# Kernel optimization log

Measured on AMD Instinct MI355X. Metric: run time of the kernel, lower is better.

The kernel has to match this reference:

```python
import jax, jax.numpy as jnp
import numpy as np

B, N, S = 8, 8192, 2048
D1, D2 = 128, 256
IN_CH = D1 + D2  # 384
MLP = [256, 128]
BN_EPS = 1e-5


def setup_inputs() -> dict:
    key = jax.random.key(0)
    ks = jax.random.split(key, 12)
    inp = {
        'xyz1': jax.random.normal(ks[0], (B, 3, N), dtype=jnp.float32),
        'xyz2': jax.random.normal(ks[1], (B, 3, S), dtype=jnp.float32),
        'points1': jax.random.normal(ks[2], (B, D1, N), dtype=jnp.float32),
        'points2': jax.random.normal(ks[3], (B, D2, S), dtype=jnp.float32),
    }
    # Conv1d(kernel=1) weights [out, in] + bias, BN gamma/beta per layer
    c_in = IN_CH
    for i, c_out in enumerate(MLP):
        scale = 1.0 / np.sqrt(c_in)
        inp[f'w{i}'] = jax.random.uniform(ks[4 + 2 * i], (c_out, c_in), jnp.float32, -scale, scale)
        inp[f'b{i}'] = jax.random.uniform(ks[5 + 2 * i], (c_out,), jnp.float32, -scale, scale)
        inp[f'g{i}'] = jnp.ones((c_out,), jnp.float32)
        inp[f'be{i}'] = jnp.zeros((c_out,), jnp.float32)
        c_in = c_out
    return inp


def _fp_forward(xyz1, xyz2, points1, points2, params):
    # xyz1: [B,3,N] -> [B,N,3]; xyz2: [B,3,S] -> [B,S,3]
    p1 = jnp.transpose(xyz1, (0, 2, 1))
    p2 = jnp.transpose(xyz2, (0, 2, 1))
    # squared pairwise distances [B,N,S]
    dist = (jnp.sum(p1 * p1, -1)[:, :, None]
            + jnp.sum(p2 * p2, -1)[:, None, :]
            - 2.0 * jnp.einsum('bnc,bsc->bns', p1, p2))
    # 3 smallest distances per query point
    neg_d, idx = jax.lax.top_k(-dist, 3)          # idx: [B,N,3]
    d3 = -neg_d
    recip = 1.0 / (d3 + 1e-8)
    weight = recip / jnp.sum(recip, axis=2, keepdims=True)  # [B,N,3]
    # gather neighbor features: points2 [B,D2,S] -> [B,S,D2]
    feats = jnp.transpose(points2, (0, 2, 1))
    gathered = feats[jnp.arange(feats.shape[0])[:, None, None], idx]  # [B,N,3,D2]
    interp = jnp.einsum('bnkd,bnk->bdn', gathered, weight)            # [B,D2,N]
    x = jnp.concatenate([points1, interp], axis=1)                    # [B,D1+D2,N]
    # Conv1d(k=1) + BatchNorm1d(train-mode batch stats) + ReLU stack
    for w, b, g, be in params:
        x = jnp.einsum('oc,bcn->bon', w, x) + b[None, :, None]
        mean = jnp.mean(x, axis=(0, 2), keepdims=True)
        var = jnp.mean((x - mean) ** 2, axis=(0, 2), keepdims=True)
        x = (x - mean) * jax.lax.rsqrt(var + BN_EPS)
        x = x * g[None, :, None] + be[None, :, None]
        x = jax.nn.relu(x)
    return x


def reference(xyz1, xyz2, points1, points2, w0, b0, g0, be0, w1, b1, g1, be1):
    params = [(w0, b0, g0, be0), (w1, b1, g1, be1)]
    return _fp_forward(xyz1, xyz2, points1, points2, params)
```

## Files before the change

kernel.cpp:

```cpp
#include <hip/hip_runtime.h>

#define NB   8
#define NPT  8192
#define NS   2048
#define ND1  128
#define ND2  256
#define NIN  384
#define NC0  256
#define NC1  128
#define NBN  (NB*NPT)

typedef __bf16 bf16x8 __attribute__((ext_vector_type(8)));
typedef __bf16 bf16x4 __attribute__((ext_vector_type(4)));
typedef float  f32x4  __attribute__((ext_vector_type(4)));

__global__ __launch_bounds__(256) void knn_kernel(
    const float* __restrict__ xyz1, const float* __restrict__ xyz2,
    int* __restrict__ idx3, float* __restrict__ wgt3)
{
    __shared__ float4 pts[NS];
    __shared__ float md[64][4][3];
    __shared__ int   mi[64][4][3];

    const int b  = blockIdx.x;
    const int qt = blockIdx.y;
    const float* x2 = xyz2 + (size_t)b * 3 * NS;
    for (int s = threadIdx.x; s < NS; s += 256) {
        float x = x2[s], y = x2[NS + s], z = x2[2 * NS + s];
        pts[s] = make_float4(x, y, z, x * x + y * y + z * z);
    }
    __syncthreads();

    const int q    = threadIdx.x & 63;
    const int part = threadIdx.x >> 6;
    const int n    = qt * 64 + q;
    const float* x1 = xyz1 + (size_t)b * 3 * NPT;
    const float px = x1[n], py = x1[NPT + n], pz = x1[2 * NPT + n];

    float d0 = 3e38f, d1 = 3e38f, d2 = 3e38f;
    int   i0 = 0, i1 = 0, i2 = 0;
    const int sbeg = part * (NS / 4);
    #pragma unroll 2
    for (int s = sbeg; s < sbeg + NS / 4; ++s) {
        float4 p = pts[s];
        float t = px * p.x;
        t = fmaf(py, p.y, t);
        t = fmaf(pz, p.z, t);
        float d = fmaf(-2.f, t, p.w);
        bool c0 = d < d0, c1 = d < d1, c2 = d < d2;
        i2 = c1 ? i1 : (c2 ? s : i2);
        i1 = c0 ? i0 : (c1 ? s : i1);
        i0 = c0 ? s  : i0;
        d2 = fminf(fmaxf(d, d1), d2);
        d1 = fminf(fmaxf(d, d0), d1);
        d0 = fminf(d, d0);
    }
    md[q][part][0] = d0; md[q][part][1] = d1; md[q][part][2] = d2;
    mi[q][part][0] = i0; mi[q][part][1] = i1; mi[q][part][2] = i2;
    __syncthreads();

    if (threadIdx.x < 64) {
        int hp[4] = {0, 0, 0, 0};
        float rd[3]; int ri[3];
        #pragma unroll
        for (int k = 0; k < 3; ++k) {
            float best = 3.0e38f; int bl = 0;
            #pragma unroll
            for (int l = 0; l < 4; ++l) {
                float dv = md[q][l][hp[l]];
                if (dv < best) { best = dv; bl = l; }
            }
            rd[k] = best; ri[k] = mi[q][bl][hp[bl]]; hp[bl]++;
        }
        const float p1sq = px * px + py * py + pz * pz;
        float r0 = 1.0f / (rd[0] + p1sq + 1e-8f);
        float r1 = 1.0f / (rd[1] + p1sq + 1e-8f);
        float r2 = 1.0f / (rd[2] + p1sq + 1e-8f);
        float inv = 1.0f / (r0 + r1 + r2);
        size_t base = ((size_t)b * NPT + n) * 3;
        idx3[base] = ri[0]; idx3[base + 1] = ri[1]; idx3[base + 2] = ri[2];
        wgt3[base] = r0 * inv; wgt3[base + 1] = r1 * inv; wgt3[base + 2] = r2 * inv;
    }
}

__global__ __launch_bounds__(256) void transpose_p2_kernel(
    const float* __restrict__ p2, __bf16* __restrict__ p2t)
{
    __shared__ float tile[64][65];
    const int b  = blockIdx.x;
    const int ts = (blockIdx.y & 31) * 64;
    const int td = (blockIdx.y >> 5) * 64;
    const int sl = threadIdx.x & 63, dl = threadIdx.x >> 6;
    #pragma unroll
    for (int i = 0; i < 16; ++i)
        tile[dl + 4 * i][sl] = p2[((size_t)b * ND2 + td + dl + 4 * i) * NS + ts + sl];
    __syncthreads();
    const int dl2 = threadIdx.x & 63, sl2 = threadIdx.x >> 6;
    #pragma unroll
    for (int i = 0; i < 16; ++i)
        p2t[((size_t)b * NS + ts + sl2 + 4 * i) * ND2 + td + dl2] =
            (__bf16)tile[dl2][sl2 + 4 * i];
}

__global__ __launch_bounds__(256) void build_xc_kernel(
    const float* __restrict__ points1, const __bf16* __restrict__ p2t,
    const int* __restrict__ idx3, const float* __restrict__ wgt3,
    __bf16* __restrict__ Xc)
{
    const int b = blockIdx.x;
    const int n = blockIdx.y * 256 + threadIdx.x;
    const size_t base3 = ((size_t)b * NPT + n) * 3;
    const int i0 = idx3[base3], i1 = idx3[base3 + 1], i2 = idx3[base3 + 2];
    const float w0 = wgt3[base3], w1 = wgt3[base3 + 1], w2 = wgt3[base3 + 2];

    __bf16* dst = Xc + ((size_t)b * NPT + n) * NIN;
    const float* p1 = points1 + (size_t)b * ND1 * NPT + n;
    #pragma unroll 2
    for (int c0 = 0; c0 < ND1; c0 += 8) {
        bf16x8 v;
        #pragma unroll
        for (int j = 0; j < 8; ++j) v[j] = (__bf16)p1[(size_t)(c0 + j) * NPT];
        *(bf16x8*)(dst + c0) = v;
    }
    const __bf16* r0 = p2t + ((size_t)b * NS + i0) * ND2;
    const __bf16* r1 = p2t + ((size_t)b * NS + i1) * ND2;
    const __bf16* r2 = p2t + ((size_t)b * NS + i2) * ND2;
    #pragma unroll 2
    for (int d0 = 0; d0 < ND2; d0 += 8) {
        bf16x8 a = *(const bf16x8*)(r0 + d0);
        bf16x8 c = *(const bf16x8*)(r1 + d0);
        bf16x8 e = *(const bf16x8*)(r2 + d0);
        bf16x8 v;
        #pragma unroll
        for (int j = 0; j < 8; ++j)
            v[j] = (__bf16)(w0 * (float)a[j] + w1 * (float)c[j] + w2 * (float)e[j]);
        *(bf16x8*)(dst + ND1 + d0) = v;
    }
}

__global__ __launch_bounds__(256) void convert_w_kernel(
    const float* __restrict__ w0, const float* __restrict__ w1,
    __bf16* __restrict__ Wb0, __bf16* __restrict__ Wb1)
{
    const int t = blockIdx.x * 256 + threadIdx.x;
    if (t < NC0 * NIN) Wb0[t] = (__bf16)w0[t];
    if (t < NC1 * NC0) Wb1[t] = (__bf16)w1[t];
}

__global__ __launch_bounds__(512, 4) void gemm0_mfma(
    const __bf16* __restrict__ Wb, const __bf16* __restrict__ Xc,
    __bf16* __restrict__ y0, float* __restrict__ sums, float* __restrict__ sumsq)
{
    __shared__ float red[2][NC0][2];
    const int tid = threadIdx.x;
    const int l = tid & 63, w = tid >> 6;
    const int g = l >> 4, lm = l & 15;
    const int ow = w >> 1, nw = w & 1;
    const int o_base = ow * 64;
    const int n_base = blockIdx.x * 128 + nw * 64;

    f32x4 acc[4][4] = {};

    for (int k0 = 0; k0 < NIN; k0 += 32) {
        const int kk = k0 + g * 8;
        bf16x8 af[4], bfr[4];
        #pragma unroll
        for (int m = 0; m < 4; ++m)
            af[m] = *(const bf16x8*)&Wb[(size_t)(o_base + m * 16 + lm) * NIN + kk];
        #pragma unroll
        for (int r = 0; r < 4; ++r)
            bfr[r] = *(const bf16x8*)&Xc[(size_t)(n_base + r * 16 + lm) * NIN + kk];
        #pragma unroll
        for (int m = 0; m < 4; ++m)
            #pragma unroll
            for (int r = 0; r < 4; ++r)
                acc[m][r] = __builtin_amdgcn_mfma_f32_16x16x32_bf16(af[m], bfr[r], acc[m][r], 0, 0, 0);
    }

    #pragma unroll
    for (int m = 0; m < 4; ++m) {
        float s[4] = {0.f, 0.f, 0.f, 0.f}, q[4] = {0.f, 0.f, 0.f, 0.f};
        #pragma unroll
        for (int r = 0; r < 4; ++r) {
            const int n = n_base + r * 16 + lm;
            bf16x4 pk;
            #pragma unroll
            for (int j = 0; j < 4; ++j) {
                float v = acc[m][r][j];
                pk[j] = (__bf16)v;
                s[j] += v; q[j] += v * v;
            }
            *(bf16x4*)&y0[(size_t)n * NC0 + o_base + m * 16 + g * 4] = pk;
        }
        #pragma unroll
        for (int j = 0; j < 4; ++j) {
            #pragma unroll
            for (int st = 1; st < 16; st <<= 1) {
                s[j] += __shfl_xor(s[j], st);
                q[j] += __shfl_xor(q[j], st);
            }
        }
        if (lm == 0) {
            #pragma unroll
            for (int j = 0; j < 4; ++j) {
                red[0][o_base + m * 16 + g * 4 + j][nw] = s[j];
                red[1][o_base + m * 16 + g * 4 + j][nw] = q[j];
            }
        }
    }
    __syncthreads();
    if (tid < NC0) {
        atomicAdd(&sums[tid],  red[0][tid][0] + red[0][tid][1]);
        atomicAdd(&sumsq[tid], red[1][tid][0] + red[1][tid][1]);
    }
}

__global__ void stats_kernel(
    const float* __restrict__ sums, const float* __restrict__ sumsq,
    const float* __restrict__ g, const float* __restrict__ be,
    float* __restrict__ scale, float* __restrict__ shift, int C)
{
    int c = blockIdx.x * blockDim.x + threadIdx.x;
    if (c < C) {
        const float invN = 1.0f / (float)NBN;
        float mean = sums[c] * invN;
        float var  = sumsq[c] * invN - mean * mean;
        float sc   = g[c] * rsqrtf(var + 1e-5f);
        scale[c] = sc;
        shift[c] = be[c] - mean * sc;
    }
}

__global__ __launch_bounds__(512, 4) void gemm1_mfma(
    const __bf16* __restrict__ Wb, const __bf16* __restrict__ y0,
    const float* __restrict__ scale0, const float* __restrict__ shift0,
    __bf16* __restrict__ y1, float* __restrict__ sums, float* __restrict__ sumsq)
{
    __shared__ float red[2][NC1][4];
    const int tid = threadIdx.x;
    const int l = tid & 63, w = tid >> 6;
    const int g = l >> 4, lm = l & 15;
    const int ow = w >> 2, nw = w & 3;
    const int o_base = ow * 64;
    const int n_base = blockIdx.x * 128 + nw * 32;

    f32x4 acc[4][2] = {};

    for (int k0 = 0; k0 < NC0; k0 += 32) {
        const int kk = k0 + g * 8;
        f32x4 sc0 = *(const f32x4*)&scale0[kk];
        f32x4 sc1 = *(const f32x4*)&scale0[kk + 4];
        f32x4 sh0 = *(const f32x4*)&shift0[kk];
        f32x4 sh1 = *(const f32x4*)&shift0[kk + 4];
        bf16x8 af[4], bfr[2];
        #pragma unroll
        for (int m = 0; m < 4; ++m)
            af[m] = *(const bf16x8*)&Wb[(size_t)(o_base + m * 16 + lm) * NC0 + kk];
        #pragma unroll
        for (int r = 0; r < 2; ++r) {
            bf16x8 raw = *(const bf16x8*)&y0[(size_t)(n_base + r * 16 + lm) * NC0 + kk];
            bf16x8 bb;
            #pragma unroll
            for (int j = 0; j < 4; ++j) {
                bb[j]     = (__bf16)fmaxf((float)raw[j]     * sc0[j] + sh0[j], 0.f);
                bb[j + 4] = (__bf16)fmaxf((float)raw[j + 4] * sc1[j] + sh1[j], 0.f);
            }
            bfr[r] = bb;
        }
        #pragma unroll
        for (int m = 0; m < 4; ++m)
            #pragma unroll
            for (int r = 0; r < 2; ++r)
                acc[m][r] = __builtin_amdgcn_mfma_f32_16x16x32_bf16(af[m], bfr[r], acc[m][r], 0, 0, 0);
    }

    #pragma unroll
    for (int m = 0; m < 4; ++m) {
        float s[4] = {0.f, 0.f, 0.f, 0.f}, q[4] = {0.f, 0.f, 0.f, 0.f};
        #pragma unroll
        for (int r = 0; r < 2; ++r) {
            const int n = n_base + r * 16 + lm;
            #pragma unroll
            for (int j = 0; j < 4; ++j) {
                float v = acc[m][r][j];
                y1[(size_t)(o_base + m * 16 + g * 4 + j) * NBN + n] = (__bf16)v;
                s[j] += v; q[j] += v * v;
            }
        }
        #pragma unroll
        for (int j = 0; j < 4; ++j) {
            #pragma unroll
            for (int st = 1; st < 16; st <<= 1) {
                s[j] += __shfl_xor(s[j], st);
                q[j] += __shfl_xor(q[j], st);
            }
        }
        if (lm == 0) {
            #pragma unroll
            for (int j = 0; j < 4; ++j) {
                red[0][o_base + m * 16 + g * 4 + j][nw] = s[j];
                red[1][o_base + m * 16 + g * 4 + j][nw] = q[j];
            }
        }
    }
    __syncthreads();
    if (tid < NC1) {
        atomicAdd(&sums[tid],  red[0][tid][0] + red[0][tid][1] + red[0][tid][2] + red[0][tid][3]);
        atomicAdd(&sumsq[tid], red[1][tid][0] + red[1][tid][1] + red[1][tid][2] + red[1][tid][3]);
    }
}

__global__ __launch_bounds__(256) void bnout_kernel(
    const __bf16* __restrict__ y1, const float* __restrict__ scale1,
    const float* __restrict__ shift1, float* __restrict__ out)
{
    const size_t t = (size_t)blockIdx.x * 256 + threadIdx.x;
    const size_t e = t * 8;
    const int n = (int)(e & (NPT - 1));
    const int o = (int)((e >> 13) & (NC1 - 1));
    const int b = (int)(e >> 20);
    bf16x8 v = *(const bf16x8*)&y1[(size_t)o * NBN + (size_t)b * NPT + n];
    const float s = scale1[o], sh = shift1[o];
    f32x4 r0, r1;
    #pragma unroll
    for (int j = 0; j < 4; ++j) {
        r0[j] = fmaxf((float)v[j]     * s + sh, 0.f);
        r1[j] = fmaxf((float)v[j + 4] * s + sh, 0.f);
    }
    *(f32x4*)&out[e]     = r0;
    *(f32x4*)&out[e + 4] = r1;
}

extern "C" void kernel_launch(void* const* d_in, const int* in_sizes, int n_in,
                              void* d_out, int out_size, void* d_ws, size_t ws_size,
                              hipStream_t stream)
{
    const float* xyz1    = (const float*)d_in[0];
    const float* xyz2    = (const float*)d_in[1];
    const float* points1 = (const float*)d_in[2];
    const float* points2 = (const float*)d_in[3];
    const float* w0  = (const float*)d_in[4];
    const float* g0  = (const float*)d_in[6];
    const float* be0 = (const float*)d_in[7];
    const float* w1  = (const float*)d_in[8];
    const float* g1  = (const float*)d_in[10];
    const float* be1 = (const float*)d_in[11];

    char* ws = (char*)d_ws;
    size_t off = 0;
    int*    idx3 = (int*)(ws + off);    off += (size_t)NBN * 3 * 4;
    float*  wgt3 = (float*)(ws + off);  off += (size_t)NBN * 3 * 4;
    __bf16* Xc   = (__bf16*)(ws + off); off += (size_t)NBN * NIN * 2;
    __bf16* y0   = (__bf16*)(ws + off); off += (size_t)NBN * NC0 * 2;
    __bf16* y1   = (__bf16*)(ws + off); off += (size_t)NC1 * NBN * 2;
    __bf16* p2t  = (__bf16*)(ws + off); off += (size_t)NB * NS * ND2 * 2;
    __bf16* Wb0  = (__bf16*)(ws + off); off += (size_t)NC0 * NIN * 2;
    __bf16* Wb1  = (__bf16*)(ws + off); off += (size_t)NC1 * NC0 * 2;
    float*  stats = (float*)(ws + off);
    float* sums0  = stats;        float* sumsq0 = stats + 256;
    float* sums1  = stats + 512;  float* sumsq1 = stats + 640;
    float* scale0 = stats + 768;  float* shift0 = stats + 1024;
    float* scale1 = stats + 1280; float* shift1 = stats + 1408;

    hipMemsetAsync(stats, 0, 768 * 4, stream);

    convert_w_kernel   <<<dim3(NC0 * NIN / 256), 256, 0, stream>>>(w0, w1, Wb0, Wb1);
    transpose_p2_kernel<<<dim3(NB, 128), 256, 0, stream>>>(points2, p2t);
    knn_kernel         <<<dim3(NB, 128), 256, 0, stream>>>(xyz1, xyz2, idx3, wgt3);
    build_xc_kernel    <<<dim3(NB, NPT / 256), 256, 0, stream>>>(points1, p2t, idx3, wgt3, Xc);
    gemm0_mfma         <<<dim3(NBN / 128), 512, 0, stream>>>(Wb0, Xc, y0, sums0, sumsq0);
    stats_kernel       <<<1, 256, 0, stream>>>(sums0, sumsq0, g0, be0, scale0, shift0, NC0);
    gemm1_mfma         <<<dim3(NBN / 128), 512, 0, stream>>>(Wb1, y0, scale0, shift0, y1, sums1, sumsq1);
    stats_kernel       <<<1, 128, 0, stream>>>(sums1, sumsq1, g1, be1, scale1, shift1, NC1);
    bnout_kernel       <<<dim3(NBN * NC1 / 8 / 256), 256, 0, stream>>>(y1, scale1, shift1, (float*)d_out);
}
```

Measured before the change: 337.3 us.

## Register-block two queries per KNN thread and move points1 transpose to tiled kernel

The KNN kernel now has each thread handle two query points across 8 source partitions. Each shared-memory point load is reused for two distance evaluations, and v_med3 is used to update the top-3. The partial results are reduced through the reused point buffer. The points1 part of the concatenated input is now written by a separate LDS-tiled transpose kernel instead of strided per-thread reads in build_xc, which is meant to coalesce the global reads. The cost is an extra kernel launch and a wider 8-way merge.

```diff
diff --git a/kernel.cpp b/kernel.cpp
--- a/kernel.cpp
+++ b/kernel.cpp
@@ -19,8 +19,6 @@
     int* __restrict__ idx3, float* __restrict__ wgt3)
 {
     __shared__ float4 pts[NS];
-    __shared__ float md[64][4][3];
-    __shared__ int   mi[64][4][3];
 
     const int b  = blockIdx.x;
     const int qt = blockIdx.y;
@@ -31,47 +29,80 @@
     }
     __syncthreads();
 
-    const int q    = threadIdx.x & 63;
-    const int part = threadIdx.x >> 6;
-    const int n    = qt * 64 + q;
+    const int qg   = threadIdx.x & 31;
+    const int part = threadIdx.x >> 5;
+    const int n0   = qt * 64 + qg * 2;
     const float* x1 = xyz1 + (size_t)b * 3 * NPT;
-    const float px = x1[n], py = x1[NPT + n], pz = x1[2 * NPT + n];
-
-    float d0 = 3e38f, d1 = 3e38f, d2 = 3e38f;
-    int   i0 = 0, i1 = 0, i2 = 0;
-    const int sbeg = part * (NS / 4);
-    #pragma unroll 2
-    for (int s = sbeg; s < sbeg + NS / 4; ++s) {
+    const float ax = x1[n0],     ay = x1[NPT + n0],     az = x1[2 * NPT + n0];
+    const float bx = x1[n0 + 1], by = x1[NPT + n0 + 1], bz = x1[2 * NPT + n0 + 1];
+
+    float ad0 = 3e38f, ad1 = 3e38f, ad2 = 3e38f;
+    float bd0 = 3e38f, bd1 = 3e38f, bd2 = 3e38f;
+    int   ai0 = 0, ai1 = 0, ai2 = 0;
+    int   bi0 = 0, bi1 = 0, bi2 = 0;
+
+    const int sbeg = part * 256;
+    #pragma unroll 4
+    for (int s = sbeg; s < sbeg + 256; ++s) {
         float4 p = pts[s];
-        float t = px * p.x;
-        t = fmaf(py, p.y, t);
-        t = fmaf(pz, p.z, t);
-        float d = fmaf(-2.f, t, p.w);
-        bool c0 = d < d0, c1 = d < d1, c2 = d < d2;
-        i2 = c1 ? i1 : (c2 ? s : i2);
-        i1 = c0 ? i0 : (c1 ? s : i1);
-        i0 = c0 ? s  : i0;
-        d2 = fminf(fmaxf(d, d1), d2);
-        d1 = fminf(fmaxf(d, d0), d1);
-        d0 = fminf(d, d0);
-    }
-    md[q][part][0] = d0; md[q][part][1] = d1; md[q][part][2] = d2;
-    mi[q][part][0] = i0; mi[q][part][1] = i1; mi[q][part][2] = i2;
+        float ta = ax * p.x; ta = fmaf(ay, p.y, ta); ta = fmaf(az, p.z, ta);
+        float da = fmaf(-2.f, ta, p.w);
+        {
+            bool c0 = da < ad0, c1 = da < ad1, c2 = da < ad2;
+            ai2 = c1 ? ai1 : (c2 ? s : ai2);
+            ai1 = c0 ? ai0 : (c1 ? s : ai1);
+            ai0 = c0 ? s : ai0;
+            float m2, m1;
+            asm("v_med3_f32 %0, %1, %2, %3" : "=v"(m2) : "v"(da), "v"(ad1), "v"(ad2));
+            asm("v_med3_f32 %0, %1, %2, %3" : "=v"(m1) : "v"(da), "v"(ad0), "v"(ad1));
+            ad2 = m2; ad1 = m1; ad0 = fminf(da, ad0);
+        }
+        float tb = bx * p.x; tb = fmaf(by, p.y, tb); tb = fmaf(bz, p.z, tb);
+        float db = fmaf(-2.f, tb, p.w);
+        {
+            bool c0 = db < bd0, c1 = db < bd1, c2 = db < bd2;
+            bi2 = c1 ? bi1 : (c2 ? s : bi2);
+            bi1 = c0 ? bi0 : (c1 ? s : bi1);
+            bi0 = c0 ? s : bi0;
+            float m2, m1;
+            asm("v_med3_f32 %0, %1, %2, %3" : "=v"(m2) : "v"(db), "v"(bd1), "v"(bd2));
+            asm("v_med3_f32 %0, %1, %2, %3" : "=v"(m1) : "v"(db), "v"(bd0), "v"(bd1));
+            bd2 = m2; bd1 = m1; bd0 = fminf(db, bd0);
+        }
+    }
+    __syncthreads();
+
+    float* md = (float*)pts;
+    int*   mi = (int*)pts + 64 * 8 * 3;
+    {
+        const int q0 = qg * 2;
+        int base = (q0 * 8 + part) * 3;
+        md[base] = ad0; md[base + 1] = ad1; md[base + 2] = ad2;
+        mi[base] = ai0; mi[base + 1] = ai1; mi[base + 2] = ai2;
+        base += 24;
+        md[base] = bd0; md[base + 1] = bd1; md[base + 2] = bd2;
+        mi[base] = bi0; mi[base + 1] = bi1; mi[base + 2] = bi2;
+    }
     __syncthreads();
 
     if (threadIdx.x < 64) {
-        int hp[4] = {0, 0, 0, 0};
+        const int q = threadIdx.x;
+        const int n = qt * 64 + q;
+        int hp[8] = {0, 0, 0, 0, 0, 0, 0, 0};
         float rd[3]; int ri[3];
         #pragma unroll
         for (int k = 0; k < 3; ++k) {
             float best = 3.0e38f; int bl = 0;
             #pragma unroll
-            for (int l = 0; l < 4; ++l) {
-                float dv = md[q][l][hp[l]];
+            for (int l = 0; l < 8; ++l) {
+                float dv = md[(q * 8 + l) * 3 + hp[l]];
                 if (dv < best) { best = dv; bl = l; }
             }
-            rd[k] = best; ri[k] = mi[q][bl][hp[bl]]; hp[bl]++;
-        }
+            rd[k] = best; ri[k] = mi[(q * 8 + bl) * 3 + hp[bl]];
+            #pragma unroll
+            for (int l = 0; l < 8; ++l) if (l == bl) hp[l]++;
+        }
+        const float px = x1[n], py = x1[NPT + n], pz = x1[2 * NPT + n];
         const float p1sq = px * px + py * py + pz * pz;
         float r0 = 1.0f / (rd[0] + p1sq + 1e-8f);
         float r1 = 1.0f / (rd[1] + p1sq + 1e-8f);
@@ -102,8 +133,32 @@
             (__bf16)tile[dl2][sl2 + 4 * i];
 }
 
+__global__ __launch_bounds__(256) void transpose_p1_kernel(
+    const float* __restrict__ p1, __bf16* __restrict__ Xc)
+{
+    __shared__ float tile[64][65];
+    const int b  = blockIdx.x;
+    const int tn = (blockIdx.y & 127) * 64;
+    const int tc = (blockIdx.y >> 7) * 64;
+    const int sl = threadIdx.x & 63, dl = threadIdx.x >> 6;
+    #pragma unroll
+    for (int i = 0; i < 16; ++i)
+        tile[dl + 4 * i][sl] = p1[((size_t)b * ND1 + tc + dl + 4 * i) * NPT + tn + sl];
+    __syncthreads();
+    const int n_local = threadIdx.x >> 2, c16 = threadIdx.x & 3;
+    __bf16* dst = Xc + ((size_t)b * NPT + tn + n_local) * NIN + tc + c16 * 16;
+    bf16x8 v0, v1;
+    #pragma unroll
+    for (int k = 0; k < 8; ++k) {
+        v0[k] = (__bf16)tile[c16 * 16 + k][n_local];
+        v1[k] = (__bf16)tile[c16 * 16 + 8 + k][n_local];
+    }
+    *(bf16x8*)dst = v0;
+    *(bf16x8*)(dst + 8) = v1;
+}
+
 __global__ __launch_bounds__(256) void build_xc_kernel(
-    const float* __restrict__ points1, const __bf16* __restrict__ p2t,
+    const __bf16* __restrict__ p2t,
     const int* __restrict__ idx3, const float* __restrict__ wgt3,
     __bf16* __restrict__ Xc)
 {
@@ -114,14 +169,6 @@
     const float w0 = wgt3[base3], w1 = wgt3[base3 + 1], w2 = wgt3[base3 + 2];
 
     __bf16* dst = Xc + ((size_t)b * NPT + n) * NIN;
-    const float* p1 = points1 + (size_t)b * ND1 * NPT + n;
-    #pragma unroll 2
-    for (int c0 = 0; c0 < ND1; c0 += 8) {
-        bf16x8 v;
-        #pragma unroll
-        for (int j = 0; j < 8; ++j) v[j] = (__bf16)p1[(size_t)(c0 + j) * NPT];
-        *(bf16x8*)(dst + c0) = v;
-    }
     const __bf16* r0 = p2t + ((size_t)b * NS + i0) * ND2;
     const __bf16* r1 = p2t + ((size_t)b * NS + i1) * ND2;
     const __bf16* r2 = p2t + ((size_t)b * NS + i2) * ND2;
@@ -366,8 +413,9 @@
 
     convert_w_kernel   <<<dim3(NC0 * NIN / 256), 256, 0, stream>>>(w0, w1, Wb0, Wb1);
     transpose_p2_kernel<<<dim3(NB, 128), 256, 0, stream>>>(points2, p2t);
+    transpose_p1_kernel<<<dim3(NB, 256), 256, 0, stream>>>(points1, Xc);
     knn_kernel         <<<dim3(NB, 128), 256, 0, stream>>>(xyz1, xyz2, idx3, wgt3);
-    build_xc_kernel    <<<dim3(NB, NPT / 256), 256, 0, stream>>>(points1, p2t, idx3, wgt3, Xc);
+    build_xc_kernel    <<<dim3(NB, NPT / 256), 256, 0, stream>>>(p2t, idx3, wgt3, Xc);
     gemm0_mfma         <<<dim3(NBN / 128), 512, 0, stream>>>(Wb0, Xc, y0, sums0, sumsq0);
     stats_kernel       <<<1, 256, 0, stream>>>(sums0, sumsq0, g0, be0, scale0, shift0, NC0);
     gemm1_mfma         <<<dim3(NBN / 128), 512, 0, stream>>>(Wb1, y0, scale0, shift0, y1, sums1, sumsq1);
```

Measured after the change: 342.2 us. About the same (+1.5%).

## Fuse neighbor interpolation into first GEMM via swizzled LDS tile

Applied to the files above, without the earlier changes.

Removes the separate build_xc kernel and the full Xc buffer in global memory. The first GEMM now builds its 64-point activation tile directly in swizzled shared memory: it takes points1 from a new coalesced transpose kernel and interpolates the three gathered neighbor rows inside the block. This saves one write and one read of a large bf16 intermediate. The cost is a halved GEMM tile per block (64 points instead of 128), more blocks, 48KB of LDS, and the gather latency now sitting in the GEMM prologue. The KNN distance is also folded into a three-fma chain with a pre-scaled query.

```diff
diff --git a/kernel.cpp b/kernel.cpp
--- a/kernel.cpp
+++ b/kernel.cpp
@@ -14,6 +14,8 @@
 typedef __bf16 bf16x4 __attribute__((ext_vector_type(4)));
 typedef float  f32x4  __attribute__((ext_vector_type(4)));
 
+#define SWZ(n, off) ((off) ^ (((n) & 7) << 4))
+
 __global__ __launch_bounds__(256) void knn_kernel(
     const float* __restrict__ xyz1, const float* __restrict__ xyz2,
     int* __restrict__ idx3, float* __restrict__ wgt3)
@@ -36,6 +38,7 @@
     const int n    = qt * 64 + q;
     const float* x1 = xyz1 + (size_t)b * 3 * NPT;
     const float px = x1[n], py = x1[NPT + n], pz = x1[2 * NPT + n];
+    const float qx = -2.f * px, qy = -2.f * py, qz = -2.f * pz;
 
     float d0 = 3e38f, d1 = 3e38f, d2 = 3e38f;
     int   i0 = 0, i1 = 0, i2 = 0;
@@ -43,10 +46,7 @@
     #pragma unroll 2
     for (int s = sbeg; s < sbeg + NS / 4; ++s) {
         float4 p = pts[s];
-        float t = px * p.x;
-        t = fmaf(py, p.y, t);
-        t = fmaf(pz, p.z, t);
-        float d = fmaf(-2.f, t, p.w);
+        float d = fmaf(qx, p.x, fmaf(qy, p.y, fmaf(qz, p.z, p.w)));
         bool c0 = d < d0, c1 = d < d1, c2 = d < d2;
         i2 = c1 ? i1 : (c2 ? s : i2);
         i1 = c0 ? i0 : (c1 ? s : i1);
@@ -102,40 +102,28 @@
             (__bf16)tile[dl2][sl2 + 4 * i];
 }
 
-__global__ __launch_bounds__(256) void build_xc_kernel(
-    const float* __restrict__ points1, const __bf16* __restrict__ p2t,
-    const int* __restrict__ idx3, const float* __restrict__ wgt3,
-    __bf16* __restrict__ Xc)
-{
-    const int b = blockIdx.x;
-    const int n = blockIdx.y * 256 + threadIdx.x;
-    const size_t base3 = ((size_t)b * NPT + n) * 3;
-    const int i0 = idx3[base3], i1 = idx3[base3 + 1], i2 = idx3[base3 + 2];
-    const float w0 = wgt3[base3], w1 = wgt3[base3 + 1], w2 = wgt3[base3 + 2];
-
-    __bf16* dst = Xc + ((size_t)b * NPT + n) * NIN;
-    const float* p1 = points1 + (size_t)b * ND1 * NPT + n;
-    #pragma unroll 2
-    for (int c0 = 0; c0 < ND1; c0 += 8) {
-        bf16x8 v;
-        #pragma unroll
-        for (int j = 0; j < 8; ++j) v[j] = (__bf16)p1[(size_t)(c0 + j) * NPT];
-        *(bf16x8*)(dst + c0) = v;
-    }
-    const __bf16* r0 = p2t + ((size_t)b * NS + i0) * ND2;
-    const __bf16* r1 = p2t + ((size_t)b * NS + i1) * ND2;
-    const __bf16* r2 = p2t + ((size_t)b * NS + i2) * ND2;
-    #pragma unroll 2
-    for (int d0 = 0; d0 < ND2; d0 += 8) {
-        bf16x8 a = *(const bf16x8*)(r0 + d0);
-        bf16x8 c = *(const bf16x8*)(r1 + d0);
-        bf16x8 e = *(const bf16x8*)(r2 + d0);
-        bf16x8 v;
-        #pragma unroll
-        for (int j = 0; j < 8; ++j)
-            v[j] = (__bf16)(w0 * (float)a[j] + w1 * (float)c[j] + w2 * (float)e[j]);
-        *(bf16x8*)(dst + ND1 + d0) = v;
-    }
+__global__ __launch_bounds__(256) void transpose_p1_kernel(
+    const float* __restrict__ p1, __bf16* __restrict__ XcP1)
+{
+    __shared__ float tile[64][65];
+    const int b  = blockIdx.x;
+    const int tn = (blockIdx.y & 127) * 64;
+    const int tc = (blockIdx.y >> 7) * 64;
+    const int sl = threadIdx.x & 63, dl = threadIdx.x >> 6;
+    #pragma unroll
+    for (int i = 0; i < 16; ++i)
+        tile[dl + 4 * i][sl] = p1[((size_t)b * ND1 + tc + dl + 4 * i) * NPT + tn + sl];
+    __syncthreads();
+    const int n_local = threadIdx.x >> 2, c16 = threadIdx.x & 3;
+    __bf16* dst = XcP1 + ((size_t)b * NPT + tn + n_local) * ND1 + tc + c16 * 16;
+    bf16x8 v0, v1;
+    #pragma unroll
+    for (int k = 0; k < 8; ++k) {
+        v0[k] = (__bf16)tile[c16 * 16 + k][n_local];
+        v1[k] = (__bf16)tile[c16 * 16 + 8 + k][n_local];
+    }
+    *(bf16x8*)dst = v0;
+    *(bf16x8*)(dst + 8) = v1;
 }
 
 __global__ __launch_bounds__(256) void convert_w_kernel(
@@ -147,33 +135,75 @@
     if (t < NC1 * NC0) Wb1[t] = (__bf16)w1[t];
 }
 
-__global__ __launch_bounds__(512, 4) void gemm0_mfma(
-    const __bf16* __restrict__ Wb, const __bf16* __restrict__ Xc,
+__global__ __launch_bounds__(512, 4) void gemm0_fused(
+    const __bf16* __restrict__ Wb, const __bf16* __restrict__ XcP1,
+    const __bf16* __restrict__ p2t,
+    const int* __restrict__ idx3, const float* __restrict__ wgt3,
     __bf16* __restrict__ y0, float* __restrict__ sums, float* __restrict__ sumsq)
 {
+    __shared__ char BsRaw[64 * NIN * 2];
     __shared__ float red[2][NC0][2];
+    char* lds = BsRaw;
+
     const int tid = threadIdx.x;
+    const int bn0 = blockIdx.x * 64;
+    const int b   = bn0 / NPT;
+
+    #pragma unroll
+    for (int i = 0; i < 2; ++i) {
+        const int id = tid + i * 512;
+        const int n  = id >> 4;
+        const int c8 = (id & 15) * 8;
+        bf16x8 v = *(const bf16x8*)&XcP1[(size_t)(bn0 + n) * ND1 + c8];
+        *(bf16x8*)(lds + n * (NIN * 2) + SWZ(n, c8 * 2)) = v;
+    }
+
+    {
+        const int ng   = tid >> 3;
+        const int part = tid & 7;
+        const size_t base3 = (size_t)(bn0 + ng) * 3;
+        const int i0 = idx3[base3], i1 = idx3[base3 + 1], i2 = idx3[base3 + 2];
+        const float w0 = wgt3[base3], w1 = wgt3[base3 + 1], w2 = wgt3[base3 + 2];
+        const __bf16* r0 = p2t + ((size_t)b * NS + i0) * ND2;
+        const __bf16* r1 = p2t + ((size_t)b * NS + i1) * ND2;
+        const __bf16* r2 = p2t + ((size_t)b * NS + i2) * ND2;
+        #pragma unroll
+        for (int i = 0; i < 4; ++i) {
+            const int d0 = part * 32 + i * 8;
+            bf16x8 a = *(const bf16x8*)(r0 + d0);
+            bf16x8 c = *(const bf16x8*)(r1 + d0);
+            bf16x8 e = *(const bf16x8*)(r2 + d0);
+            bf16x8 v;
+            #pragma unroll
+            for (int j = 0; j < 8; ++j)
+                v[j] = (__bf16)(w0 * (float)a[j] + w1 * (float)c[j] + w2 * (float)e[j]);
+            *(bf16x8*)(lds + ng * (NIN * 2) + SWZ(ng, (ND1 + d0) * 2)) = v;
+        }
+    }
+    __syncthreads();
+
     const int l = tid & 63, w = tid >> 6;
     const int g = l >> 4, lm = l & 15;
     const int ow = w >> 1, nw = w & 1;
     const int o_base = ow * 64;
-    const int n_base = blockIdx.x * 128 + nw * 64;
-
-    f32x4 acc[4][4] = {};
+
+    f32x4 acc[4][2] = {};
 
     for (int k0 = 0; k0 < NIN; k0 += 32) {
         const int kk = k0 + g * 8;
-        bf16x8 af[4], bfr[4];
+        bf16x8 af[4], bfr[2];
         #pragma unroll
         for (int m = 0; m < 4; ++m)
             af[m] = *(const bf16x8*)&Wb[(size_t)(o_base + m * 16 + lm) * NIN + kk];
         #pragma unroll
-        for (int r = 0; r < 4; ++r)
-            bfr[r] = *(const bf16x8*)&Xc[(size_t)(n_base + r * 16 + lm) * NIN + kk];
+        for (int r = 0; r < 2; ++r) {
+            const int n_lds = nw * 32 + r * 16 + lm;
+            bfr[r] = *(const bf16x8*)(lds + n_lds * (NIN * 2) + SWZ(n_lds, kk * 2));
+        }
         #pragma unroll
         for (int m = 0; m < 4; ++m)
             #pragma unroll
-            for (int r = 0; r < 4; ++r)
+            for (int r = 0; r < 2; ++r)
                 acc[m][r] = __builtin_amdgcn_mfma_f32_16x16x32_bf16(af[m], bfr[r], acc[m][r], 0, 0, 0);
     }
 
@@ -181,8 +211,8 @@
     for (int m = 0; m < 4; ++m) {
         float s[4] = {0.f, 0.f, 0.f, 0.f}, q[4] = {0.f, 0.f, 0.f, 0.f};
         #pragma unroll
-        for (int r = 0; r < 4; ++r) {
-            const int n = n_base + r * 16 + lm;
+        for (int r = 0; r < 2; ++r) {
+            const int n = nw * 32 + r * 16 + lm;
             bf16x4 pk;
             #pragma unroll
             for (int j = 0; j < 4; ++j) {
@@ -190,7 +220,7 @@
                 pk[j] = (__bf16)v;
                 s[j] += v; q[j] += v * v;
             }
-            *(bf16x4*)&y0[(size_t)n * NC0 + o_base + m * 16 + g * 4] = pk;
+            *(bf16x4*)&y0[(size_t)(bn0 + n) * NC0 + o_base + m * 16 + g * 4] = pk;
         }
         #pragma unroll
         for (int j = 0; j < 4; ++j) {
@@ -350,7 +380,7 @@
     size_t off = 0;
     int*    idx3 = (int*)(ws + off);    off += (size_t)NBN * 3 * 4;
     float*  wgt3 = (float*)(ws + off);  off += (size_t)NBN * 3 * 4;
-    __bf16* Xc   = (__bf16*)(ws + off); off += (size_t)NBN * NIN * 2;
+    __bf16* XcP1 = (__bf16*)(ws + off); off += (size_t)NBN * ND1 * 2;
     __bf16* y0   = (__bf16*)(ws + off); off += (size_t)NBN * NC0 * 2;
     __bf16* y1   = (__bf16*)(ws + off); off += (size_t)NC1 * NBN * 2;
     __bf16* p2t  = (__bf16*)(ws + off); off += (size_t)NB * NS * ND2 * 2;
@@ -366,9 +396,10 @@
 
     convert_w_kernel   <<<dim3(NC0 * NIN / 256), 256, 0, stream>>>(w0, w1, Wb0, Wb1);
     transpose_p2_kernel<<<dim3(NB, 128), 256, 0, stream>>>(points2, p2t);
+    transpose_p1_kernel<<<dim3(NB, 256), 256, 0, stream>>>(points1, XcP1);
     knn_kernel         <<<dim3(NB, 128), 256, 0, stream>>>(xyz1, xyz2, idx3, wgt3);
-    build_xc_kernel    <<<dim3(NB, NPT / 256), 256, 0, stream>>>(points1, p2t, idx3, wgt3, Xc);
-    gemm0_mfma         <<<dim3(NBN / 128), 512, 0, stream>>>(Wb0, Xc, y0, sums0, sumsq0);
+    gemm0_fused        <<<dim3(NBN / 64), 512, 0, stream>>>(
+        Wb0, XcP1, p2t, idx3, wgt3, y0, sums0, sumsq0);
     stats_kernel       <<<1, 256, 0, stream>>>(sums0, sumsq0, g0, be0, scale0, shift0, NC0);
     gemm1_mfma         <<<dim3(NBN / 128), 512, 0, stream>>>(Wb1, y0, scale0, shift0, y1, sums1, sumsq1);
     stats_kernel       <<<1, 128, 0, stream>>>(sums1, sumsq1, g1, be1, scale1, shift1, NC1);
```

New measurement: 328.9 us. 1.03x faster.
